# Performance work log

Measured on AMD Instinct MI355X. Metric: run time of the kernel, lower is better.

## Reference

```python
import jax, jax.numpy as jnp
import numpy as np

EPS_CLAMP = 1e-6
TAU2 = 1.0


def _l2norm_rows(x):
    # F.normalize(x, p=2, dim=1) with eps=1e-12
    n = jnp.sqrt(jnp.sum(x * x, axis=1, keepdims=True))
    return x / jnp.maximum(n, 1e-12)


def _ws_v22(x_mean, x_std):
    m = _l2norm_rows(x_mean)                      # [N, F]
    c = _l2norm_rows(jnp.exp(x_std))              # [N, F]
    sq = jnp.sum(m * m, axis=1)                   # [N]
    # squared euclidean pairwise distance (cdist(...)**2)
    d2 = jnp.maximum(sq[:, None] + sq[None, :] - 2.0 * (m @ m.T), 0.0)
    csum = jnp.sum(c, axis=1)                     # [N]
    cs = jnp.sqrt(c)
    res = d2 + csum[:, None] + csum[None, :] - 2.0 * (cs @ cs.T)
    return jnp.exp(-res)                          # [N, N]


def _gcn_conv_dense(A, x, W, b):
    # PyG GCNConv with dense weighted adjacency A (A[i,j] = weight of edge i->j),
    # add_remaining_self_loops(fill=1), deg over target (column sums),
    # norm_ij = d_i^-1/2 * A_ij * d_j^-1/2, aggregate at target: out = A_norm^T @ (xW) + b
    diag = jnp.diagonal(A)
    A = A + jnp.diag(jnp.where(diag > 0, 0.0, 1.0))  # add self-loop weight 1 only where missing
    deg = jnp.sum(A, axis=0)                         # column sums (target degree)
    dis = jnp.where(deg > 0, deg ** -0.5, 0.0)
    An = dis[:, None] * A * dis[None, :]
    return An.T @ (x @ W) + b


def _encoder(A, x, W0, b0, W1, b1):
    h = jax.nn.relu(_gcn_conv_dense(A, x, W0, b0))
    return jax.nn.relu(_gcn_conv_dense(A, h, W1, b1))


def setup_inputs() -> dict:
    key = jax.random.key(0)
    ks = jax.random.split(key, 16)
    N, F, H = 4096, 512, 256
    s_in = 1.0 / np.sqrt(F)
    s_h = 1.0 / np.sqrt(2 * H)
    inp = {
        "x": jax.random.normal(ks[0], (N, F), dtype=jnp.float32),
        "new_edge": jax.random.uniform(ks[1], (N, N), dtype=jnp.float32),
        "beta": jax.random.uniform(ks[2], (1,), dtype=jnp.float32),
        "delta": jax.random.uniform(ks[3], (1,), dtype=jnp.float32),
        "eps": jax.random.uniform(ks[4], (N, N), dtype=jnp.float32),
        "Wm": jax.random.uniform(ks[5], (F, F), jnp.float32, -s_in, s_in),
        "bm": jax.random.uniform(ks[6], (F,), jnp.float32, -s_in, s_in),
        "Ws": jax.random.uniform(ks[7], (F, F), jnp.float32, -s_in, s_in),
        "bs": jax.random.uniform(ks[8], (F,), jnp.float32, -s_in, s_in),
        "mW0": jax.random.uniform(ks[9], (F, 2 * H), jnp.float32, -s_in, s_in) ,
        "mb0": jnp.zeros((2 * H,), jnp.float32),
        "mW1": jax.random.uniform(ks[10], (2 * H, H), jnp.float32, -s_h, s_h),
        "mb1": jnp.zeros((H,), jnp.float32),
        "sW0": jax.random.uniform(ks[11], (F, 2 * H), jnp.float32, -s_in, s_in),
        "sb0": jnp.zeros((2 * H,), jnp.float32),
        "sW1": jax.random.uniform(ks[12], (2 * H, H), jnp.float32, -s_h, s_h),
        "sb1": jnp.zeros((H,), jnp.float32),
    }
    return inp


def reference(x, new_edge, beta, delta, eps, Wm, bm, Ws, bs,
              mW0, mb0, mW1, mb1, sW0, sb0, sW1, sb1):
    b = beta[0]
    d = delta[0]
    x_mean = x @ Wm + bm
    x_std = x @ Ws + bs
    ws = _l2norm_rows(_ws_v22(x_mean, x_std))       # F.normalize(WS_v22(...)) row-wise
    term = (1.0 - b) * ws + b * new_edge
    term = jnp.clip(term, EPS_CLAMP, 1.0 - EPS_CLAMP)
    term = jnp.log(term / (1.0 - term))
    e = jnp.clip(eps, EPS_CLAMP, 1.0 - EPS_CLAMP)
    term = term + jnp.log(e / (1.0 - e))
    term = jax.nn.sigmoid(term / TAU2)
    term = jnp.where(term > d, term, 0.0)           # dense sparsified adjacency
    z_mean = _encoder(term, x_mean, mW0, mb0, mW1, mb1)
    z_std = _encoder(term, x_std, sW0, sb0, sW1, sb1)
    return z_mean, z_std
```

## Files before the change

kernel.cpp:

```cpp
#include <hip/hip_runtime.h>
#include <cstddef>

static constexpr int kN = 4096;
static constexpr int kF = 512;
static constexpr int kH = 256;
static constexpr float kClamp = 1e-6f;

using bf16x8 = __attribute__((ext_vector_type(8))) __bf16;
using f32x4 = __attribute__((ext_vector_type(4))) float;
using ushort8 = __attribute__((ext_vector_type(8))) unsigned short;
using ushort4v = __attribute__((ext_vector_type(4))) unsigned short;

static constexpr size_t PLANE_XF = (size_t)kN * kF;
static constexpr size_t PLANE_NN = (size_t)kN * kN;
static constexpr size_t PLANE_W = (size_t)512 * 512;
static constexpr size_t PLANE_W1 = (size_t)256 * 512;
static constexpr size_t PLANE_V0 = (size_t)1024 * kN;
static constexpr size_t PLANE_H = (size_t)kN * 1024;
static constexpr size_t PLANE_V1 = (size_t)512 * kN;

__device__ __forceinline__ unsigned short f2bf(float x) {
  unsigned int u = __float_as_uint(x);
  u += 0x7fffu + ((u >> 16) & 1u);
  return (unsigned short)(u >> 16);
}
__device__ __forceinline__ float bf2f(unsigned short h) {
  return __uint_as_float(((unsigned int)h) << 16);
}
__device__ __forceinline__ void split3(float x, unsigned short& h,
                                       unsigned short& m, unsigned short& l) {
  h = f2bf(x);
  const float r1 = x - bf2f(h);
  m = f2bf(r1);
  l = f2bf(r1 - bf2f(m));
}
__device__ __forceinline__ void split2(float x, unsigned short& h,
                                       unsigned short& m) {
  h = f2bf(x);
  m = f2bf(x - bf2f(h));
}
__device__ __forceinline__ void split3x4(const float4 v, ushort4v& h4,
                                         ushort4v& m4, ushort4v& l4) {
  unsigned short h, m, l;
  split3(v.x, h, m, l); h4.x = h; m4.x = m; l4.x = l;
  split3(v.y, h, m, l); h4.y = h; m4.y = m; l4.y = l;
  split3(v.z, h, m, l); h4.z = h; m4.z = m; l4.z = l;
  split3(v.w, h, m, l); h4.w = h; m4.w = m; l4.w = l;
}
__device__ __forceinline__ void split2x4(const float4 v, ushort4v& h4,
                                         ushort4v& m4) {
  unsigned short h, m;
  split2(v.x, h, m); h4.x = h; m4.x = m;
  split2(v.y, h, m); h4.y = h; m4.y = m;
  split2(v.z, h, m); h4.z = h; m4.z = m;
  split2(v.w, h, m); h4.w = h; m4.w = m;
}

__device__ __forceinline__ bf16x8 ldfrag(const unsigned short* p) {
  ushort8 r = *(const ushort8*)p;
  return __builtin_bit_cast(bf16x8, r);
}
__device__ __forceinline__ f32x4 mfma16(bf16x8 a, bf16x8 b, f32x4 c) {
  return __builtin_amdgcn_mfma_f32_16x16x32_bf16(a, b, c, 0, 0, 0);
}
__device__ __forceinline__ f32x4 mfma_split6(const bf16x8* a3, const bf16x8* b3,
                                             f32x4 acc) {
  acc = mfma16(a3[2], b3[0], acc);
  acc = mfma16(a3[0], b3[2], acc);
  acc = mfma16(a3[1], b3[1], acc);
  acc = mfma16(a3[1], b3[0], acc);
  acc = mfma16(a3[0], b3[1], acc);
  acc = mfma16(a3[0], b3[0], acc);
  return acc;
}

__device__ __forceinline__ void tri_map(int b, int& bi, int& bj) {
  int x = (int)((sqrtf(8.0f * (float)b + 1.0f) - 1.0f) * 0.5f);
  while ((x + 1) * (x + 2) / 2 <= b) ++x;
  while (x * (x + 1) / 2 > b) --x;
  bi = x;
  bj = b - x * (x + 1) / 2;
}

__device__ __forceinline__ float block_reduce_sum(float v, float* sbuf) {
  const int tid = threadIdx.x;
  sbuf[tid] = v;
  __syncthreads();
#pragma unroll
  for (int s = 128; s > 0; s >>= 1) {
    if (tid < s) sbuf[tid] += sbuf[tid + s];
    __syncthreads();
  }
  const float r = sbuf[0];
  __syncthreads();
  return r;
}

__global__ __launch_bounds__(256) void prep_w(
    const float* s0, const float* s1, const float* s2, const float* s3,
    const float* s4, const float* s5, unsigned short* d0, unsigned short* d1,
    unsigned short* d2, unsigned short* d3, unsigned short* d4,
    unsigned short* d5) {
  const int seg = blockIdx.y;
  const float* src;
  unsigned short* dst;
  int N;
  bool tri;
  switch (seg) {
    case 0: src = s0; dst = d0; N = 512; tri = true; break;
    case 1: src = s1; dst = d1; N = 512; tri = true; break;
    case 2: src = s2; dst = d2; N = 512; tri = false; break;
    case 3: src = s3; dst = d3; N = 512; tri = false; break;
    case 4: src = s4; dst = d4; N = 256; tri = false; break;
    default: src = s5; dst = d5; N = 256; tri = false; break;
  }
  const int id = blockIdx.x * 256 + threadIdx.x;
  if (id >= 512 * N) return;
  const int k = id & 511;
  const int n = id >> 9;
  const float v = src[(size_t)k * N + n];
  const size_t base = (size_t)n * 512 + k;
  const size_t plane = (size_t)512 * N;
  if (tri) {
    unsigned short h, m, l;
    split3(v, h, m, l);
    dst[base] = h;
    dst[plane + base] = m;
    dst[2 * plane + base] = l;
  } else {
    unsigned short h, m;
    split2(v, h, m);
    dst[base] = h;
    dst[plane + base] = m;
  }
}

__global__ __launch_bounds__(256) void split_x(const float* __restrict__ x,
                                               unsigned short* __restrict__ x3) {
  const size_t id = (size_t)blockIdx.x * 256 + threadIdx.x;
  unsigned short h, m, l;
  split3(x[id], h, m, l);
  x3[id] = h;
  x3[PLANE_XF + id] = m;
  x3[2 * PLANE_XF + id] = l;
}

__global__ __launch_bounds__(256) void gemm_x(
    const unsigned short* __restrict__ A3, const unsigned short* __restrict__ B30,
    const unsigned short* __restrict__ B31, float* __restrict__ C0,
    float* __restrict__ C1, const float* __restrict__ bias0,
    const float* __restrict__ bias1) {
  constexpr int BM = 128, BN = 64, K = 512;
  __shared__ __align__(16) unsigned short Asl[3][BM][40];
  __shared__ __align__(16) unsigned short Bsl[3][BN][40];
  const int tid = threadIdx.x;
  const int lane = tid & 63;
  const int wave = tid >> 6;
  const int wm = wave >> 1, wn = wave & 1;
  const int m0 = blockIdx.y * BM;
  const int n0 = blockIdx.x * BN;
  const bool str1 = (n0 >= 512);
  const int nloc = str1 ? (n0 - 512) : n0;
  const unsigned short* Bb = str1 ? B31 : B30;
  const float* bias = str1 ? bias1 : bias0;
  float* C = str1 ? C1 : C0;
  const int rl = lane & 15;
  const int kq = (lane >> 4) * 8;
  const int q = lane >> 4;

  f32x4 acc[4][2];
#pragma unroll
  for (int i = 0; i < 4; ++i)
#pragma unroll
    for (int j = 0; j < 2; ++j) acc[i][j] = (f32x4){0.f, 0.f, 0.f, 0.f};

  for (int k0 = 0; k0 < K; k0 += 32) {
#pragma unroll
    for (int it = 0; it < 6; ++it) {
      const int c = tid + it * 256;
      const int plane = c / (BM * 4);
      const int rem = c % (BM * 4);
      const int row = rem >> 2;
      const int kc = (rem & 3) * 8;
      const ushort8 v = *(const ushort8*)(&A3[(size_t)plane * PLANE_XF +
                                              (size_t)(m0 + row) * K + k0 + kc]);
      *(ushort8*)(&Asl[plane][row][kc]) = v;
    }
#pragma unroll
    for (int it = 0; it < 3; ++it) {
      const int c = tid + it * 256;
      const int plane = c / (BN * 4);
      const int rem = c % (BN * 4);
      const int row = rem >> 2;
      const int kc = (rem & 3) * 8;
      const ushort8 v = *(const ushort8*)(&Bb[(size_t)plane * PLANE_W +
                                              (size_t)(nloc + row) * K + k0 + kc]);
      *(ushort8*)(&Bsl[plane][row][kc]) = v;
    }
    __syncthreads();
    bf16x8 af[4][3], bfr[2][3];
#pragma unroll
    for (int mt = 0; mt < 4; ++mt)
#pragma unroll
      for (int t = 0; t < 3; ++t)
        af[mt][t] = ldfrag(&Asl[t][wm * 64 + mt * 16 + rl][kq]);
#pragma unroll
    for (int nt = 0; nt < 2; ++nt)
#pragma unroll
      for (int t = 0; t < 3; ++t)
        bfr[nt][t] = ldfrag(&Bsl[t][wn * 32 + nt * 16 + rl][kq]);
#pragma unroll
    for (int mt = 0; mt < 4; ++mt)
#pragma unroll
      for (int nt = 0; nt < 2; ++nt)
        acc[mt][nt] = mfma_split6(af[mt], bfr[nt], acc[mt][nt]);
    __syncthreads();
  }
#pragma unroll
  for (int mt = 0; mt < 4; ++mt)
#pragma unroll
    for (int nt = 0; nt < 2; ++nt) {
      const int col = nloc + wn * 32 + nt * 16 + rl;
      const int row0 = m0 + wm * 64 + mt * 16 + q * 4;
      const float bv = bias[col];
#pragma unroll
      for (int r = 0; r < 4; ++r)
        C[(size_t)(row0 + r) * 512 + col] = acc[mt][nt][r] + bv;
    }
}

template <int BM, int BN, int OUT, int NP>
__global__ __launch_bounds__(256) void gemm2(
    const unsigned short* __restrict__ A0, const unsigned short* __restrict__ A1,
    int lda, size_t planeA, const unsigned short* __restrict__ B0,
    const unsigned short* __restrict__ B1, int ldb, size_t planeB,
    unsigned short* __restrict__ Cs0, unsigned short* __restrict__ Cs1,
    float* __restrict__ Cp, int ldc, size_t planeC, int N1, int K,
    const float* __restrict__ rowScale) {
  __shared__ __align__(16) unsigned short Asl[2][BM][40];
  __shared__ __align__(16) unsigned short Bsl[2][BN][40];
  const int tid = threadIdx.x;
  const int lane = tid & 63;
  const int wave = tid >> 6;
  const int wm = wave >> 1, wn = wave & 1;
  const int m0 = blockIdx.y * BM;
  const int n0 = blockIdx.x * BN;
  const int kOff = blockIdx.z * K;
  const bool str1 = (n0 >= N1);
  const int nloc = str1 ? (n0 - N1) : n0;
  const unsigned short* Ab = str1 ? A1 : A0;
  const unsigned short* Bb = str1 ? B1 : B0;
  const int rl = lane & 15;
  const int kq = (lane >> 4) * 8;
  const int q = lane >> 4;
  constexpr int MT = BM / 32;
  constexpr int NT = BN / 32;

  f32x4 acc[MT][NT];
#pragma unroll
  for (int i = 0; i < MT; ++i)
#pragma unroll
    for (int j = 0; j < NT; ++j) acc[i][j] = (f32x4){0.f, 0.f, 0.f, 0.f};

  for (int k0 = 0; k0 < K; k0 += 32) {
    constexpr int AIT = (2 * BM * 4) / 256;
#pragma unroll
    for (int it = 0; it < AIT; ++it) {
      const int c = tid + it * 256;
      const int plane = c / (BM * 4);
      const int rem = c % (BM * 4);
      const int row = rem >> 2;
      const int kc = (rem & 3) * 8;
      const ushort8 v = *(const ushort8*)(&Ab[(size_t)plane * planeA +
                                              (size_t)(m0 + row) * lda + kOff +
                                              k0 + kc]);
      *(ushort8*)(&Asl[plane][row][kc]) = v;
    }
    constexpr int BIT = (2 * BN * 4) / 256;
#pragma unroll
    for (int it = 0; it < BIT; ++it) {
      const int c = tid + it * 256;
      const int plane = c / (BN * 4);
      const int rem = c % (BN * 4);
      const int row = rem >> 2;
      const int kc = (rem & 3) * 8;
      const ushort8 v = *(const ushort8*)(&Bb[(size_t)plane * planeB +
                                              (size_t)(nloc + row) * ldb + kOff +
                                              k0 + kc]);
      *(ushort8*)(&Bsl[plane][row][kc]) = v;
    }
    __syncthreads();
    bf16x8 af[MT][2];
#pragma unroll
    for (int mt = 0; mt < MT; ++mt)
#pragma unroll
      for (int t = 0; t < 2; ++t)
        af[mt][t] = ldfrag(&Asl[t][wm * (BM / 2) + mt * 16 + rl][kq]);
#pragma unroll
    for (int nt = 0; nt < NT; ++nt) {
      const bf16x8 b0 = ldfrag(&Bsl[0][wn * (BN / 2) + nt * 16 + rl][kq]);
      const bf16x8 b1 = ldfrag(&Bsl[1][wn * (BN / 2) + nt * 16 + rl][kq]);
#pragma unroll
      for (int mt = 0; mt < MT; ++mt) {
        if (NP == 4) acc[mt][nt] = mfma16(af[mt][1], b1, acc[mt][nt]);
        acc[mt][nt] = mfma16(af[mt][1], b0, acc[mt][nt]);
        acc[mt][nt] = mfma16(af[mt][0], b1, acc[mt][nt]);
        acc[mt][nt] = mfma16(af[mt][0], b0, acc[mt][nt]);
      }
    }
    __syncthreads();
  }

#pragma unroll
  for (int mt = 0; mt < MT; ++mt) {
#pragma unroll
    for (int nt = 0; nt < NT; ++nt) {
      const int colL = nloc + wn * (BN / 2) + nt * 16 + rl;
      const int row0 = m0 + wm * (BM / 2) + mt * 16 + q * 4;
      if (OUT == 2) {
        float4 v4;
        float* vp = &v4.x;
#pragma unroll
        for (int r = 0; r < 4; ++r) {
          float v = acc[mt][nt][r];
          if (rowScale) v *= rowScale[row0 + r];
          vp[r] = v;
        }
        unsigned short* C = str1 ? Cs1 : Cs0;
        ushort4v h4, m4;
        split2x4(v4, h4, m4);
        const size_t base = (size_t)colL * ldc + row0;
        *(ushort4v*)(&C[base]) = h4;
        *(ushort4v*)(&C[planeC + base]) = m4;
      } else {
        const size_t zoff =
            (size_t)blockIdx.z * (size_t)(gridDim.y * BM) * (size_t)ldc;
#pragma unroll
        for (int r = 0; r < 4; ++r)
          Cp[zoff + (size_t)(row0 + r) * ldc + colL] = acc[mt][nt][r];
      }
    }
  }
}

__global__ __launch_bounds__(256) void row_stats(
    const float* __restrict__ XMf, const float* __restrict__ XSf,
    unsigned short* __restrict__ M2, unsigned short* __restrict__ CS2,
    unsigned short* __restrict__ XM2, unsigned short* __restrict__ XS2,
    float* __restrict__ sq, float* __restrict__ csum) {
  __shared__ float sbuf[256];
  const int i = blockIdx.x;
  const int tid = threadIdx.x;
  const size_t base = (size_t)i * kF;
  const size_t i0 = base + tid, i1 = base + tid + 256;
  const float x0 = XMf[i0], x1 = XMf[i1];
  {
    unsigned short h, m;
    split2(x0, h, m);
    XM2[i0] = h; XM2[PLANE_XF + i0] = m;
    split2(x1, h, m);
    XM2[i1] = h; XM2[PLANE_XF + i1] = m;
  }
  const float nrm = block_reduce_sum(x0 * x0 + x1 * x1, sbuf);
  const float inv = 1.0f / fmaxf(sqrtf(nrm), 1e-12f);
  const float m0 = x0 * inv, m1 = x1 * inv;
  {
    unsigned short h, m;
    split2(m0, h, m);
    M2[i0] = h; M2[PLANE_XF + i0] = m;
    split2(m1, h, m);
    M2[i1] = h; M2[PLANE_XF + i1] = m;
  }
  const float s2 = block_reduce_sum(m0 * m0 + m1 * m1, sbuf);
  if (tid == 0) sq[i] = s2;

  const float y0 = XSf[i0], y1 = XSf[i1];
  {
    unsigned short h, m;
    split2(y0, h, m);
    XS2[i0] = h; XS2[PLANE_XF + i0] = m;
    split2(y1, h, m);
    XS2[i1] = h; XS2[PLANE_XF + i1] = m;
  }
  const float e0 = expf(y0), e1 = expf(y1);
  const float nrm2 = block_reduce_sum(e0 * e0 + e1 * e1, sbuf);
  const float inv2 = 1.0f / fmaxf(sqrtf(nrm2), 1e-12f);
  const float c0 = e0 * inv2, c1 = e1 * inv2;
  const float sc = block_reduce_sum(c0 + c1, sbuf);
  if (tid == 0) csum[i] = sc;
  {
    unsigned short h, m;
    split2(sqrtf(c0), h, m);
    CS2[i0] = h; CS2[PLANE_XF + i0] = m;
    split2(sqrtf(c1), h, m);
    CS2[i1] = h; CS2[PLANE_XF + i1] = m;
  }
}

__global__ __launch_bounds__(256) void ws_mfma2(
    const unsigned short* __restrict__ M2, const unsigned short* __restrict__ CS2,
    const float* __restrict__ sq, const float* __restrict__ csum,
    float* __restrict__ WSR) {
  __shared__ __align__(16) unsigned short S[4][2][64][40];
  int bi, bj;
  tri_map(blockIdx.x, bi, bj);
  const int i0 = bi * 64, j0 = bj * 64;
  const int tid = threadIdx.x;
  const int lane = tid & 63;
  const int wave = tid >> 6;
  const int wm = wave >> 1, wn = wave & 1;
  const int rl = lane & 15;
  const int kq = (lane >> 4) * 8;
  const int q = lane >> 4;

  f32x4 aM[2][2], aC[2][2];
#pragma unroll
  for (int i = 0; i < 2; ++i)
#pragma unroll
    for (int j = 0; j < 2; ++j) {
      aM[i][j] = (f32x4){0.f, 0.f, 0.f, 0.f};
      aC[i][j] = (f32x4){0.f, 0.f, 0.f, 0.f};
    }

  for (int k0 = 0; k0 < kF; k0 += 32) {
#pragma unroll
    for (int it = 0; it < 8; ++it) {
      const int c = tid + it * 256;
      const int op = c >> 9;
      const int rem = c & 511;
      const int plane = rem >> 8;
      const int r2 = rem & 255;
      const int row = r2 >> 2;
      const int kc = (r2 & 3) * 8;
      const unsigned short* mat = (op & 1) ? CS2 : M2;
      const int rowoff = (op < 2) ? i0 : j0;
      const ushort8 v = *(const ushort8*)(&mat[(size_t)plane * PLANE_XF +
                                               (size_t)(rowoff + row) * kF + k0 +
                                               kc]);
      *(ushort8*)(&S[op][plane][row][kc]) = v;
    }
    __syncthreads();
    bf16x8 am[2][2], ac[2][2], bm[2][2], bc[2][2];
#pragma unroll
    for (int mt = 0; mt < 2; ++mt)
#pragma unroll
      for (int t = 0; t < 2; ++t) {
        am[mt][t] = ldfrag(&S[0][t][wm * 32 + mt * 16 + rl][kq]);
        ac[mt][t] = ldfrag(&S[1][t][wm * 32 + mt * 16 + rl][kq]);
      }
#pragma unroll
    for (int nt = 0; nt < 2; ++nt)
#pragma unroll
      for (int t = 0; t < 2; ++t) {
        bm[nt][t] = ldfrag(&S[2][t][wn * 32 + nt * 16 + rl][kq]);
        bc[nt][t] = ldfrag(&S[3][t][wn * 32 + nt * 16 + rl][kq]);
      }
#pragma unroll
    for (int mt = 0; mt < 2; ++mt)
#pragma unroll
      for (int nt = 0; nt < 2; ++nt) {
        aM[mt][nt] = mfma16(am[mt][1], bm[nt][0], aM[mt][nt]);
        aM[mt][nt] = mfma16(am[mt][0], bm[nt][1], aM[mt][nt]);
        aM[mt][nt] = mfma16(am[mt][0], bm[nt][0], aM[mt][nt]);
        aC[mt][nt] = mfma16(ac[mt][1], bc[nt][0], aC[mt][nt]);
        aC[mt][nt] = mfma16(ac[mt][0], bc[nt][1], aC[mt][nt]);
        aC[mt][nt] = mfma16(ac[mt][0], bc[nt][0], aC[mt][nt]);
      }
    __syncthreads();
  }

#pragma unroll
  for (int mt = 0; mt < 2; ++mt) {
#pragma unroll
    for (int nt = 0; nt < 2; ++nt) {
      const int j = j0 + wn * 32 + nt * 16 + rl;
      const int ib = i0 + wm * 32 + mt * 16 + q * 4;
      const float sqj = sq[j], csj = csum[j];
      float4 vv;
      float* vp = &vv.x;
#pragma unroll
      for (int r = 0; r < 4; ++r) {
        const int i = ib + r;
        const float d2 = fmaxf(sq[i] + sqj - 2.0f * aM[mt][nt][r], 0.0f);
        const float res = d2 + csum[i] + csj - 2.0f * aC[mt][nt][r];
        const float v = expf(-res);
        vp[r] = v;
        WSR[(size_t)i * kN + j] = v;
      }
      if (bi != bj) *(float4*)(&WSR[(size_t)j * kN + ib]) = vv;
    }
  }
}

__global__ __launch_bounds__(256) void row_invnorm_kernel(
    const float* __restrict__ WSR, float* __restrict__ invn) {
  __shared__ float sbuf[256];
  const int i = blockIdx.x;
  const int tid = threadIdx.x;
  const float4* rp = (const float4*)(WSR + (size_t)i * kN);
  float s = 0.0f;
#pragma unroll
  for (int q = 0; q < (kN / 4) / 256; ++q) {
    const float4 v = rp[tid + q * 256];
    s += v.x * v.x + v.y * v.y + v.z * v.z + v.w * v.w;
  }
  s = block_reduce_sum(s, sbuf);
  if (tid == 0) invn[i] = 1.0f / fmaxf(sqrtf(s), 1e-12f);
}

__device__ __forceinline__ float adj_val(float w, float inv, float nev, float ev,
                                         float b, float d, bool diag) {
  float t = (1.0f - b) * (w * inv) + b * nev;
  t = fminf(fmaxf(t, kClamp), 1.0f - kClamp);
  float L = logf(t / (1.0f - t));
  const float e = fminf(fmaxf(ev, kClamp), 1.0f - kClamp);
  L += logf(e / (1.0f - e));
  const float s = 1.0f / (1.0f + expf(-L));
  float v = (s > d) ? s : 0.0f;
  if (diag) v = (v > 0.0f) ? v : 1.0f;
  return v;
}

__global__ __launch_bounds__(256) void adj_transpose(
    const float* __restrict__ WSR, const float* __restrict__ invn,
    const float* __restrict__ ne, const float* __restrict__ epsm,
    const float* __restrict__ beta_p, const float* __restrict__ delta_p,
    unsigned short* __restrict__ Adj2, float* __restrict__ degp) {
  __shared__ float T0[64][65];
  __shared__ float T1[64][65];
  const float b = beta_p[0];
  const float d = delta_p[0];
  int bi, bj;
  tri_map(blockIdx.x, bi, bj);
  const int i0 = bi * 64, j0 = bj * 64;
  const int tid = threadIdx.x;
  const int rlq = tid >> 4;
  const int cq = (tid & 15) * 4;
#pragma unroll
  for (int p = 0; p < 4; ++p) {
    const int ii = p * 16 + rlq;
    {
      const size_t off = (size_t)(i0 + ii) * kN + j0 + cq;
      const float4 w4 = *(const float4*)(&WSR[off]);
      const float4 n4 = *(const float4*)(&ne[off]);
      const float4 e4 = *(const float4*)(&epsm[off]);
      const float inv = invn[i0 + ii];
      const float wv[4] = {w4.x, w4.y, w4.z, w4.w};
      const float nv[4] = {n4.x, n4.y, n4.z, n4.w};
      const float ev[4] = {e4.x, e4.y, e4.z, e4.w};
#pragma unroll
      for (int u = 0; u < 4; ++u)
        T0[ii][cq + u] =
            adj_val(wv[u], inv, nv[u], ev[u], b, d, (i0 + ii) == (j0 + cq + u));
    }
    if (bi != bj) {
      const size_t off = (size_t)(j0 + ii) * kN + i0 + cq;
      const float4 w4 = *(const float4*)(&WSR[off]);
      const float4 n4 = *(const float4*)(&ne[off]);
      const float4 e4 = *(const float4*)(&epsm[off]);
      const float inv = invn[j0 + ii];
      const float wv[4] = {w4.x, w4.y, w4.z, w4.w};
      const float nv[4] = {n4.x, n4.y, n4.z, n4.w};
      const float ev[4] = {e4.x, e4.y, e4.z, e4.w};
#pragma unroll
      for (int u = 0; u < 4; ++u)
        T1[ii][cq + u] = adj_val(wv[u], inv, nv[u], ev[u], b, d, false);
    }
  }
  __syncthreads();
#pragma unroll
  for (int p = 0; p < 4; ++p) {
    const int jj = p * 16 + rlq;
    {
      const float4 v4 = make_float4(T0[cq + 0][jj], T0[cq + 1][jj],
                                    T0[cq + 2][jj], T0[cq + 3][jj]);
      ushort4v h4, m4;
      split2x4(v4, h4, m4);
      const size_t base = (size_t)(j0 + jj) * kN + i0 + cq;
      *(ushort4v*)(&Adj2[base]) = h4;
      *(ushort4v*)(&Adj2[PLANE_NN + base]) = m4;
    }
    if (bi != bj) {
      const float4 v4 = make_float4(T1[cq + 0][jj], T1[cq + 1][jj],
                                    T1[cq + 2][jj], T1[cq + 3][jj]);
      ushort4v h4, m4;
      split2x4(v4, h4, m4);
      const size_t base = (size_t)(i0 + jj) * kN + j0 + cq;
      *(ushort4v*)(&Adj2[base]) = h4;
      *(ushort4v*)(&Adj2[PLANE_NN + base]) = m4;
    }
  }
  if (tid < 64) {
    float s = 0.0f;
#pragma unroll 8
    for (int ii = 0; ii < 64; ++ii) s += T0[ii][tid];
    degp[(size_t)bi * kN + j0 + tid] = s;
    if (bi != bj) {
      float s1 = 0.0f;
#pragma unroll 8
      for (int ii = 0; ii < 64; ++ii) s1 += T1[ii][tid];
      degp[(size_t)bj * kN + i0 + tid] = s1;
    }
  }
}

__global__ __launch_bounds__(256) void deg_dis_kernel(
    const float* __restrict__ degp, float* __restrict__ dis) {
  const int j = blockIdx.x * 256 + threadIdx.x;
  float s = 0.0f;
#pragma unroll
  for (int c = 0; c < 64; ++c) s += degp[(size_t)c * kN + j];
  dis[j] = (s > 0.0f) ? (1.0f / sqrtf(s)) : 0.0f;
}

__global__ __launch_bounds__(256) void combine_h(
    const float* __restrict__ hp, const float* __restrict__ dis,
    const float* __restrict__ b0, const float* __restrict__ b1,
    unsigned short* __restrict__ h2) {
  const size_t qd = (size_t)blockIdx.x * 256 + threadIdx.x;
  const int m = (int)(qd >> 8);
  const int c0 = (int)(qd & 255) * 4;
  const size_t off = (size_t)m * 1024 + c0;
  const float4 s0 = *(const float4*)(&hp[off]);
  const float4 s1 = *(const float4*)(&hp[PLANE_H + off]);
  const float4 bv = (c0 < 512) ? *(const float4*)(&b0[c0])
                               : *(const float4*)(&b1[c0 - 512]);
  const float ds = dis[m];
  float4 v4;
  v4.x = fmaxf(ds * (s0.x + s1.x) + bv.x, 0.f);
  v4.y = fmaxf(ds * (s0.y + s1.y) + bv.y, 0.f);
  v4.z = fmaxf(ds * (s0.z + s1.z) + bv.z, 0.f);
  v4.w = fmaxf(ds * (s0.w + s1.w) + bv.w, 0.f);
  ushort4v h4, m4;
  split2x4(v4, h4, m4);
  *(ushort4v*)(&h2[off]) = h4;
  *(ushort4v*)(&h2[PLANE_H + off]) = m4;
}

__global__ __launch_bounds__(256) void combine_z(
    const float* __restrict__ zp, const float* __restrict__ dis,
    const float* __restrict__ b0, const float* __restrict__ b1,
    float* __restrict__ out) {
  const size_t qd = (size_t)blockIdx.x * 256 + threadIdx.x;
  const int m = (int)(qd >> 7);
  const int c0 = (int)(qd & 127) * 4;
  const size_t off = (size_t)m * 512 + c0;
  constexpr size_t PZ = (size_t)kN * 512;
  const float4 s0 = *(const float4*)(&zp[off]);
  const float4 s1 = *(const float4*)(&zp[PZ + off]);
  const float4 s2 = *(const float4*)(&zp[2 * PZ + off]);
  const float4 s3 = *(const float4*)(&zp[3 * PZ + off]);
  const float4 bv = (c0 < 256) ? *(const float4*)(&b0[c0])
                               : *(const float4*)(&b1[c0 - 256]);
  const float ds = dis[m];
  float4 v4;
  v4.x = fmaxf(ds * (s0.x + s1.x + s2.x + s3.x) + bv.x, 0.f);
  v4.y = fmaxf(ds * (s0.y + s1.y + s2.y + s3.y) + bv.y, 0.f);
  v4.z = fmaxf(ds * (s0.z + s1.z + s2.z + s3.z) + bv.z, 0.f);
  v4.w = fmaxf(ds * (s0.w + s1.w + s2.w + s3.w) + bv.w, 0.f);
  float* dst = (c0 < 256) ? &out[(size_t)m * 256 + c0]
                          : &out[(size_t)kN * 256 + (size_t)m * 256 + (c0 - 256)];
  *(float4*)dst = v4;
}

extern "C" void kernel_launch(void* const* d_in, const int* in_sizes, int n_in,
                              void* d_out, int out_size, void* d_ws,
                              size_t ws_size, hipStream_t stream) {
  const float* x = (const float*)d_in[0];
  const float* ne = (const float*)d_in[1];
  const float* beta = (const float*)d_in[2];
  const float* delta = (const float*)d_in[3];
  const float* epsm = (const float*)d_in[4];
  const float* Wm = (const float*)d_in[5];
  const float* bm = (const float*)d_in[6];
  const float* Ws = (const float*)d_in[7];
  const float* bs = (const float*)d_in[8];
  const float* mW0 = (const float*)d_in[9];
  const float* mb0 = (const float*)d_in[10];
  const float* mW1 = (const float*)d_in[11];
  const float* mb1 = (const float*)d_in[12];
  const float* sW0 = (const float*)d_in[13];
  const float* sb0 = (const float*)d_in[14];
  const float* sW1 = (const float*)d_in[15];
  const float* sb1 = (const float*)d_in[16];
  float* out = (float*)d_out;

  char* p = (char*)d_ws;
  float* WSR = (float*)p;                     p += PLANE_NN * 4;
  unsigned short* Adj2 = (unsigned short*)p;  p += 2 * PLANE_NN * 2;
  unsigned short* x3 = (unsigned short*)p;    p += 3 * PLANE_XF * 2;
  float* XMf = (float*)p;                     p += PLANE_XF * 4;
  float* XSf = (float*)p;                     p += PLANE_XF * 4;
  unsigned short* XM2 = (unsigned short*)p;   p += 2 * PLANE_XF * 2;
  unsigned short* XS2 = (unsigned short*)p;   p += 2 * PLANE_XF * 2;
  unsigned short* M2 = (unsigned short*)p;    p += 2 * PLANE_XF * 2;
  unsigned short* CS2 = (unsigned short*)p;   p += 2 * PLANE_XF * 2;
  float* hp = (float*)p;                      p += 2 * PLANE_H * 4;
  unsigned short* Wm3 = (unsigned short*)p;   p += 3 * PLANE_W * 2;
  unsigned short* Ws3 = (unsigned short*)p;   p += 3 * PLANE_W * 2;
  unsigned short* mW0t2 = (unsigned short*)p; p += 2 * PLANE_W * 2;
  unsigned short* sW0t2 = (unsigned short*)p; p += 2 * PLANE_W * 2;
  unsigned short* mW1t2 = (unsigned short*)p; p += 2 * PLANE_W1 * 2;
  unsigned short* sW1t2 = (unsigned short*)p; p += 2 * PLANE_W1 * 2;
  float* degp = (float*)p;                    p += (size_t)64 * kN * 4;
  float* sq = (float*)p;                      p += kN * 4;
  float* csum = (float*)p;                    p += kN * 4;
  float* invn = (float*)p;                    p += kN * 4;
  float* dis = (float*)p;                     p += kN * 4;

  unsigned short* V1t2 = x3;
  unsigned short* h2 = XM2;
  unsigned short* V0t2 = M2;
  float* zp = hp;

  const dim3 blk(256);
  const int nTri = (kN / 64) * (kN / 64 + 1) / 2;
  const int BIGN = 1 << 30;

  prep_w<<<dim3(1024, 6), blk, 0, stream>>>(Wm, Ws, mW0, sW0, mW1, sW1, Wm3,
                                            Ws3, mW0t2, sW0t2, mW1t2, sW1t2);
  split_x<<<(kN * kF) / 256, blk, 0, stream>>>(x, x3);

  gemm_x<<<dim3(16, 32), blk, 0, stream>>>(x3, Wm3, Ws3, XMf, XSf, bm, bs);

  row_stats<<<kN, blk, 0, stream>>>(XMf, XSf, M2, CS2, XM2, XS2, sq, csum);

  ws_mfma2<<<nTri, blk, 0, stream>>>(M2, CS2, sq, csum, WSR);

  row_invnorm_kernel<<<kN, blk, 0, stream>>>(WSR, invn);

  adj_transpose<<<nTri, blk, 0, stream>>>(WSR, invn, ne, epsm, beta, delta,
                                          Adj2, degp);
  deg_dis_kernel<<<kN / 256, blk, 0, stream>>>(degp, dis);

  gemm2<128, 64, 2, 3><<<dim3(16, 32), blk, 0, stream>>>(
      XM2, XS2, kF, PLANE_XF, mW0t2, sW0t2, kF, PLANE_W, V0t2,
      V0t2 + (size_t)512 * kN, nullptr, kN, PLANE_V0, 512, kF, dis);

  gemm2<128, 128, 3, 3><<<dim3(8, 32, 2), blk, 0, stream>>>(
      Adj2, Adj2, kN, PLANE_NN, V0t2, V0t2, kN, PLANE_V0, nullptr, nullptr, hp,
      1024, 0, BIGN, kN / 2, nullptr);
  combine_h<<<(int)(PLANE_H / 4 / 256), blk, 0, stream>>>(hp, dis, mb0, sb0, h2);

  gemm2<64, 64, 2, 3><<<dim3(8, 64), blk, 0, stream>>>(
      h2, h2 + 512, 1024, PLANE_H, mW1t2, sW1t2, kF, PLANE_W1, V1t2,
      V1t2 + (size_t)256 * kN, nullptr, kN, PLANE_V1, 256, kF, dis);

  gemm2<128, 128, 3, 3><<<dim3(4, 32, 4), blk, 0, stream>>>(
      Adj2, Adj2, kN, PLANE_NN, V1t2, V1t2, kN, PLANE_V1, nullptr, nullptr, zp,
      512, 0, BIGN, kN / 4, nullptr);
  combine_z<<<(int)((size_t)kN * 512 / 4 / 256), blk, 0, stream>>>(zp, dis, mb1,
                                                                   sb1, out);
}
```

Before: 664.8 us.

## Split-K the adjacency GEMMs with XCD-aware block mapping and reuse workspace

The two adjacency-by-features GEMMs move into a dedicated kernel with a 1D grid. It remaps block indices so that each of the 8 XCDs handles a contiguous band of output rows, which is meant to improve L2 reuse of the adjacency tiles. The first aggregation now uses split-K of 4 instead of 2, raising the block count to 1024 for better occupancy, at the cost of writing and re-reading 4 partial planes in combine_h. The partial sums are stored in the no-longer-needed WSR buffer instead of a separate allocation, and the output-conversion GEMM is split into its own specialized kernel.

```diff
diff --git a/kernel.cpp b/kernel.cpp
--- a/kernel.cpp
+++ b/kernel.cpp
@@ -38,14 +38,6 @@
                                        unsigned short& m) {
   h = f2bf(x);
   m = f2bf(x - bf2f(h));
-}
-__device__ __forceinline__ void split3x4(const float4 v, ushort4v& h4,
-                                         ushort4v& m4, ushort4v& l4) {
-  unsigned short h, m, l;
-  split3(v.x, h, m, l); h4.x = h; m4.x = m; l4.x = l;
-  split3(v.y, h, m, l); h4.y = h; m4.y = m; l4.y = l;
-  split3(v.z, h, m, l); h4.z = h; m4.z = m; l4.z = l;
-  split3(v.w, h, m, l); h4.w = h; m4.w = m; l4.w = l;
 }
 __device__ __forceinline__ void split2x4(const float4 v, ushort4v& h4,
                                          ushort4v& m4) {
@@ -229,14 +221,13 @@
     }
 }
 
-template <int BM, int BN, int OUT, int NP>
-__global__ __launch_bounds__(256) void gemm2(
+template <int BM, int BN>
+__global__ __launch_bounds__(256) void gemm2ct(
     const unsigned short* __restrict__ A0, const unsigned short* __restrict__ A1,
     int lda, size_t planeA, const unsigned short* __restrict__ B0,
     const unsigned short* __restrict__ B1, int ldb, size_t planeB,
-    unsigned short* __restrict__ Cs0, unsigned short* __restrict__ Cs1,
-    float* __restrict__ Cp, int ldc, size_t planeC, int N1, int K,
-    const float* __restrict__ rowScale) {
+    unsigned short* __restrict__ Cs0, unsigned short* __restrict__ Cs1, int ldc,
+    size_t planeC, int N1, int K, const float* __restrict__ rowScale) {
   __shared__ __align__(16) unsigned short Asl[2][BM][40];
   __shared__ __align__(16) unsigned short Bsl[2][BN][40];
   const int tid = threadIdx.x;
@@ -245,7 +236,6 @@
   const int wm = wave >> 1, wn = wave & 1;
   const int m0 = blockIdx.y * BM;
   const int n0 = blockIdx.x * BN;
-  const int kOff = blockIdx.z * K;
   const bool str1 = (n0 >= N1);
   const int nloc = str1 ? (n0 - N1) : n0;
   const unsigned short* Ab = str1 ? A1 : A0;
@@ -272,8 +262,7 @@
       const int row = rem >> 2;
       const int kc = (rem & 3) * 8;
       const ushort8 v = *(const ushort8*)(&Ab[(size_t)plane * planeA +
-                                              (size_t)(m0 + row) * lda + kOff +
-                                              k0 + kc]);
+                                              (size_t)(m0 + row) * lda + k0 + kc]);
       *(ushort8*)(&Asl[plane][row][kc]) = v;
     }
     constexpr int BIT = (2 * BN * 4) / 256;
@@ -285,8 +274,7 @@
       const int row = rem >> 2;
       const int kc = (rem & 3) * 8;
       const ushort8 v = *(const ushort8*)(&Bb[(size_t)plane * planeB +
-                                              (size_t)(nloc + row) * ldb + kOff +
-                                              k0 + kc]);
+                                              (size_t)(nloc + row) * ldb + k0 + kc]);
       *(ushort8*)(&Bsl[plane][row][kc]) = v;
     }
     __syncthreads();
@@ -302,7 +290,6 @@
       const bf16x8 b1 = ldfrag(&Bsl[1][wn * (BN / 2) + nt * 16 + rl][kq]);
 #pragma unroll
       for (int mt = 0; mt < MT; ++mt) {
-        if (NP == 4) acc[mt][nt] = mfma16(af[mt][1], b1, acc[mt][nt]);
         acc[mt][nt] = mfma16(af[mt][1], b0, acc[mt][nt]);
         acc[mt][nt] = mfma16(af[mt][0], b1, acc[mt][nt]);
         acc[mt][nt] = mfma16(af[mt][0], b0, acc[mt][nt]);
@@ -317,28 +304,117 @@
     for (int nt = 0; nt < NT; ++nt) {
       const int colL = nloc + wn * (BN / 2) + nt * 16 + rl;
       const int row0 = m0 + wm * (BM / 2) + mt * 16 + q * 4;
-      if (OUT == 2) {
-        float4 v4;
-        float* vp = &v4.x;
-#pragma unroll
-        for (int r = 0; r < 4; ++r) {
-          float v = acc[mt][nt][r];
-          if (rowScale) v *= rowScale[row0 + r];
-          vp[r] = v;
-        }
-        unsigned short* C = str1 ? Cs1 : Cs0;
-        ushort4v h4, m4;
-        split2x4(v4, h4, m4);
-        const size_t base = (size_t)colL * ldc + row0;
-        *(ushort4v*)(&C[base]) = h4;
-        *(ushort4v*)(&C[planeC + base]) = m4;
-      } else {
-        const size_t zoff =
-            (size_t)blockIdx.z * (size_t)(gridDim.y * BM) * (size_t)ldc;
-#pragma unroll
-        for (int r = 0; r < 4; ++r)
-          Cp[zoff + (size_t)(row0 + r) * ldc + colL] = acc[mt][nt][r];
+      float4 v4;
+      float* vp = &v4.x;
+#pragma unroll
+      for (int r = 0; r < 4; ++r) {
+        float v = acc[mt][nt][r];
+        if (rowScale) v *= rowScale[row0 + r];
+        vp[r] = v;
       }
+      unsigned short* C = str1 ? Cs1 : Cs0;
+      ushort4v h4, m4;
+      split2x4(v4, h4, m4);
+      const size_t base = (size_t)colL * ldc + row0;
+      *(ushort4v*)(&C[base]) = h4;
+      *(ushort4v*)(&C[planeC + base]) = m4;
+    }
+  }
+}
+
+template <int BM, int BN, int GX, int GYP, int GZ>
+__global__ __launch_bounds__(256) void gemm2k(
+    const unsigned short* __restrict__ A, int lda, size_t planeA,
+    const unsigned short* __restrict__ B, int ldb, size_t planeB,
+    float* __restrict__ Cp, int ldc, int Mtot, int Ksl) {
+  __shared__ __align__(16) unsigned short Asl[2][BM][40];
+  __shared__ __align__(16) unsigned short Bsl[2][BN][40];
+  const int lin = blockIdx.x;
+  const int xcd = lin & 7;
+  const int s = lin >> 3;
+  constexpr int per = GX * GYP;
+  const int z = s / per;
+  const int r = s - z * per;
+  const int bx = r % GX;
+  const int by = xcd * GYP + r / GX;
+  const int m0 = by * BM;
+  const int n0 = bx * BN;
+  const int kOff = z * Ksl;
+
+  const int tid = threadIdx.x;
+  const int lane = tid & 63;
+  const int wave = tid >> 6;
+  const int wm = wave >> 1, wn = wave & 1;
+  const int rl = lane & 15;
+  const int kq = (lane >> 4) * 8;
+  const int q = lane >> 4;
+  constexpr int MT = BM / 32;
+  constexpr int NT = BN / 32;
+
+  f32x4 acc[MT][NT];
+#pragma unroll
+  for (int i = 0; i < MT; ++i)
+#pragma unroll
+    for (int j = 0; j < NT; ++j) acc[i][j] = (f32x4){0.f, 0.f, 0.f, 0.f};
+
+  for (int k0 = 0; k0 < Ksl; k0 += 32) {
+    constexpr int AIT = (2 * BM * 4) / 256;
+#pragma unroll
+    for (int it = 0; it < AIT; ++it) {
+      const int c = tid + it * 256;
+      const int plane = c / (BM * 4);
+      const int rem = c % (BM * 4);
+      const int row = rem >> 2;
+      const int kc = (rem & 3) * 8;
+      const ushort8 v = *(const ushort8*)(&A[(size_t)plane * planeA +
+                                             (size_t)(m0 + row) * lda + kOff +
+                                             k0 + kc]);
+      *(ushort8*)(&Asl[plane][row][kc]) = v;
+    }
+    constexpr int BIT = (2 * BN * 4) / 256;
+#pragma unroll
+    for (int it = 0; it < BIT; ++it) {
+      const int c = tid + it * 256;
+      const int plane = c / (BN * 4);
+      const int rem = c % (BN * 4);
+      const int row = rem >> 2;
+      const int kc = (rem & 3) * 8;
+      const ushort8 v = *(const ushort8*)(&B[(size_t)plane * planeB +
+                                             (size_t)(n0 + row) * ldb + kOff +
+                                             k0 + kc]);
+      *(ushort8*)(&Bsl[plane][row][kc]) = v;
+    }
+    __syncthreads();
+    bf16x8 af[MT][2];
+#pragma unroll
+    for (int mt = 0; mt < MT; ++mt)
+#pragma unroll
+      for (int t = 0; t < 2; ++t)
+        af[mt][t] = ldfrag(&Asl[t][wm * (BM / 2) + mt * 16 + rl][kq]);
+#pragma unroll
+    for (int nt = 0; nt < NT; ++nt) {
+      const bf16x8 b0 = ldfrag(&Bsl[0][wn * (BN / 2) + nt * 16 + rl][kq]);
+      const bf16x8 b1 = ldfrag(&Bsl[1][wn * (BN / 2) + nt * 16 + rl][kq]);
+#pragma unroll
+      for (int mt = 0; mt < MT; ++mt) {
+        acc[mt][nt] = mfma16(af[mt][1], b0, acc[mt][nt]);
+        acc[mt][nt] = mfma16(af[mt][0], b1, acc[mt][nt]);
+        acc[mt][nt] = mfma16(af[mt][0], b0, acc[mt][nt]);
+      }
+    }
+    __syncthreads();
+  }
+
+  const size_t zoff = (size_t)z * (size_t)Mtot * (size_t)ldc;
+#pragma unroll
+  for (int mt = 0; mt < MT; ++mt) {
+#pragma unroll
+    for (int nt = 0; nt < NT; ++nt) {
+      const int colL = n0 + wn * (BN / 2) + nt * 16 + rl;
+      const int row0 = m0 + wm * (BM / 2) + mt * 16 + q * 4;
+#pragma unroll
+      for (int r = 0; r < 4; ++r)
+        Cp[zoff + (size_t)(row0 + r) * ldc + colL] = acc[mt][nt][r];
     }
   }
 }
@@ -623,14 +699,16 @@
   const size_t off = (size_t)m * 1024 + c0;
   const float4 s0 = *(const float4*)(&hp[off]);
   const float4 s1 = *(const float4*)(&hp[PLANE_H + off]);
+  const float4 s2 = *(const float4*)(&hp[2 * PLANE_H + off]);
+  const float4 s3 = *(const float4*)(&hp[3 * PLANE_H + off]);
   const float4 bv = (c0 < 512) ? *(const float4*)(&b0[c0])
                                : *(const float4*)(&b1[c0 - 512]);
   const float ds = dis[m];
   float4 v4;
-  v4.x = fmaxf(ds * (s0.x + s1.x) + bv.x, 0.f);
-  v4.y = fmaxf(ds * (s0.y + s1.y) + bv.y, 0.f);
-  v4.z = fmaxf(ds * (s0.z + s1.z) + bv.z, 0.f);
-  v4.w = fmaxf(ds * (s0.w + s1.w) + bv.w, 0.f);
+  v4.x = fmaxf(ds * (s0.x + s1.x + s2.x + s3.x) + bv.x, 0.f);
+  v4.y = fmaxf(ds * (s0.y + s1.y + s2.y + s3.y) + bv.y, 0.f);
+  v4.z = fmaxf(ds * (s0.z + s1.z + s2.z + s3.z) + bv.z, 0.f);
+  v4.w = fmaxf(ds * (s0.w + s1.w + s2.w + s3.w) + bv.w, 0.f);
   ushort4v h4, m4;
   split2x4(v4, h4, m4);
   *(ushort4v*)(&h2[off]) = h4;
@@ -695,7 +773,6 @@
   unsigned short* XS2 = (unsigned short*)p;   p += 2 * PLANE_XF * 2;
   unsigned short* M2 = (unsigned short*)p;    p += 2 * PLANE_XF * 2;
   unsigned short* CS2 = (unsigned short*)p;   p += 2 * PLANE_XF * 2;
-  float* hp = (float*)p;                      p += 2 * PLANE_H * 4;
   unsigned short* Wm3 = (unsigned short*)p;   p += 3 * PLANE_W * 2;
   unsigned short* Ws3 = (unsigned short*)p;   p += 3 * PLANE_W * 2;
   unsigned short* mW0t2 = (unsigned short*)p; p += 2 * PLANE_W * 2;
@@ -708,14 +785,14 @@
   float* invn = (float*)p;                    p += kN * 4;
   float* dis = (float*)p;                     p += kN * 4;
 
+  float* hp = WSR;
+  float* zp = WSR;
   unsigned short* V1t2 = x3;
   unsigned short* h2 = XM2;
   unsigned short* V0t2 = M2;
-  float* zp = hp;
 
   const dim3 blk(256);
   const int nTri = (kN / 64) * (kN / 64 + 1) / 2;
-  const int BIGN = 1 << 30;
 
   prep_w<<<dim3(1024, 6), blk, 0, stream>>>(Wm, Ws, mW0, sW0, mW1, sW1, Wm3,
                                             Ws3, mW0t2, sW0t2, mW1t2, sW1t2);
@@ -733,22 +810,20 @@
                                           Adj2, degp);
   deg_dis_kernel<<<kN / 256, blk, 0, stream>>>(degp, dis);
 
-  gemm2<128, 64, 2, 3><<<dim3(16, 32), blk, 0, stream>>>(
+  gemm2ct<128, 64><<<dim3(16, 32), blk, 0, stream>>>(
       XM2, XS2, kF, PLANE_XF, mW0t2, sW0t2, kF, PLANE_W, V0t2,
-      V0t2 + (size_t)512 * kN, nullptr, kN, PLANE_V0, 512, kF, dis);
-
-  gemm2<128, 128, 3, 3><<<dim3(8, 32, 2), blk, 0, stream>>>(
-      Adj2, Adj2, kN, PLANE_NN, V0t2, V0t2, kN, PLANE_V0, nullptr, nullptr, hp,
-      1024, 0, BIGN, kN / 2, nullptr);
+      V0t2 + (size_t)512 * kN, kN, PLANE_V0, 512, kF, dis);
+
+  gemm2k<128, 128, 8, 4, 4><<<1024, blk, 0, stream>>>(
+      Adj2, kN, PLANE_NN, V0t2, kN, PLANE_V0, hp, 1024, kN, kN / 4);
   combine_h<<<(int)(PLANE_H / 4 / 256), blk, 0, stream>>>(hp, dis, mb0, sb0, h2);
 
-  gemm2<64, 64, 2, 3><<<dim3(8, 64), blk, 0, stream>>>(
+  gemm2ct<64, 64><<<dim3(8, 64), blk, 0, stream>>>(
       h2, h2 + 512, 1024, PLANE_H, mW1t2, sW1t2, kF, PLANE_W1, V1t2,
-      V1t2 + (size_t)256 * kN, nullptr, kN, PLANE_V1, 256, kF, dis);
-
-  gemm2<128, 128, 3, 3><<<dim3(4, 32, 4), blk, 0, stream>>>(
-      Adj2, Adj2, kN, PLANE_NN, V1t2, V1t2, kN, PLANE_V1, nullptr, nullptr, zp,
-      512, 0, BIGN, kN / 4, nullptr);
+      V1t2 + (size_t)256 * kN, kN, PLANE_V1, 256, kF, dis);
+
+  gemm2k<128, 128, 4, 4, 4><<<512, blk, 0, stream>>>(
+      Adj2, kN, PLANE_NN, V1t2, kN, PLANE_V1, zp, 512, kN, kN / 4);
   combine_z<<<(int)((size_t)kN * 512 / 4 / 256), blk, 0, stream>>>(zp, dis, mb1,
                                                                    sb1, out);
 }
```

Measured after the change: 636.2 us. 1.04x faster.
